# Performance work log

Measured on AMD Instinct MI355X. Metric: run time of the kernel, lower is better.

## Reference

```python
import jax, jax.numpy as jnp
import numpy as np

B = 16        # number of lists
N = 1024      # items per list (all equal)
D = 256       # feature dim (= dim_emb, need_embedding=False)


def setup_inputs() -> dict:
    key = jax.random.key(0)
    k1, k2, k3 = jax.random.split(key, 3)
    feats = jax.random.normal(k1, (B * N, D), dtype=jnp.float32)
    length = jnp.full((B,), N, dtype=jnp.int32)
    # Bilinear params: torch nn.Bilinear(d, d, 1) -> weight [1, d, d], bias [1]
    # xavier_uniform on the 3-d weight: bound = sqrt(6 / (fan_in + fan_out)) with
    # fan_in = d (last dim), fan_out = 1*d (per torch _calculate_fan_in_and_fan_out)
    bound = float(np.sqrt(6.0 / (D + D)))
    W_upper = jax.random.uniform(k2, (1, D, D), jnp.float32, -bound, bound)
    W_lower = jax.random.uniform(k3, (1, D, D), jnp.float32, -bound, bound)
    b_upper = jnp.zeros((1,), jnp.float32)
    b_lower = jnp.zeros((1,), jnp.float32)
    return {"feats": feats, "W_upper": W_upper, "b_upper": b_upper,
            "W_lower": W_lower, "b_lower": b_lower, "length": length}


def reference(feats, W_upper, b_upper, W_lower, b_lower, length):
    # nb_layers=0, need_embedding=False -> embedding and transformer are Identity.
    b = length.shape[0]
    n = feats.shape[0] // b  # equal-length lists -> static reshape
    d = feats.shape[-1]
    X = feats.reshape(b, n, d)  # [B, n, d]
    # For list i: repeated_feats_1 row (p*n + q) = x_p, repeated_feats_2 row = x_q,
    # so adjacency[p, q] = x_p^T W x_q + bias  (Bilinear with out=1).
    upper = jnp.einsum('bnd,de,bme->bnm', X, W_upper[0], X) + b_upper[0]
    lower = jnp.einsum('bnd,de,bme->bnm', X, W_lower[0], X) + b_lower[0]
    adj = jnp.triu(upper) + jnp.tril(lower, -1)  # [B, n, n]
    return adj
```

## Files before the change

kernel.cpp:

```cpp
#include <hip/hip_runtime.h>

#define BL 16
#define NL 1024
#define DD 256
#define KSTEPS 8

typedef short bf16x8 __attribute__((ext_vector_type(8)));
typedef float f32x4 __attribute__((ext_vector_type(4)));

static __device__ __forceinline__ short f32_to_bf16(float f) {
  union { float f; unsigned u; } v; v.f = f;
  unsigned r = (v.u + 0x7FFFu + ((v.u >> 16) & 1u)) >> 16;
  return (short)r;
}

static __device__ __forceinline__ void g2l16(const short* g, short* l) {
  __builtin_amdgcn_global_load_lds(
      (const __attribute__((address_space(1))) void*)g,
      (__attribute__((address_space(3))) void*)l, 16, 0, 0);
}


static __device__ __forceinline__ void stage_tile(const short* __restrict__ gbase,
                                                  short* __restrict__ lds,
                                                  int t, int k0) {
  const int row = t >> 2, kc = t & 3;
#pragma unroll
  for (int i = 0; i < 2; ++i) {
    const short* g = gbase + (size_t)(row + 64 * i) * DD + k0 + kc * 8;
    g2l16(g, lds + i * 2048 + t * 8);
  }
}

static __device__ __forceinline__ void mma_step(const short* __restrict__ As,
                                                const short* __restrict__ Bs,
                                                int wm, int wn, int r, int quad,
                                                f32x4 acc[4][4]) {
  const int ch = (quad ^ ((r >> 1) & 3)) * 8;
  bf16x8 af[4], bf[4];
#pragma unroll
  for (int i = 0; i < 4; ++i) {
    af[i] = *(const bf16x8*)(As + (wm + i * 16 + r) * 32 + ch);
    bf[i] = *(const bf16x8*)(Bs + (wn + i * 16 + r) * 32 + ch);
  }
#pragma unroll
  for (int mt = 0; mt < 4; ++mt)
#pragma unroll
    for (int nt = 0; nt < 4; ++nt)
      acc[mt][nt] = __builtin_amdgcn_mfma_f32_16x16x32_bf16(af[mt], bf[nt], acc[mt][nt], 0, 0, 0);
}

static __device__ __forceinline__ size_t sw_off(int row, int k) {
  const int panel = k >> 5, c = (k >> 3) & 3, j = k & 7;
  const int s = (row >> 1) & 3;
  return (size_t)row * DD + panel * 32 + ((c ^ s) * 8) + j;
}

__global__ __launch_bounds__(256) void k_prep(const float* __restrict__ X,
                                              const float* __restrict__ Wu,
                                              const float* __restrict__ Wl,
                                              short* __restrict__ Xb,
                                              short* __restrict__ WTu,
                                              short* __restrict__ WTl) {
  const int bid = blockIdx.x;
  if (bid < 2048) {
    const int i = bid * 256 + threadIdx.x;
    const int row = i >> 5, c32 = i & 31;
    const int panel = c32 >> 2, c = c32 & 3;
    const float4* src = (const float4*)(X + (size_t)row * DD + panel * 32 + c * 8);
    const float4 v0 = src[0], v1 = src[1];
    short o[8] = {f32_to_bf16(v0.x), f32_to_bf16(v0.y), f32_to_bf16(v0.z), f32_to_bf16(v0.w),
                  f32_to_bf16(v1.x), f32_to_bf16(v1.y), f32_to_bf16(v1.z), f32_to_bf16(v1.w)};
    const int s = (row >> 1) & 3;
    *(bf16x8*)(Xb + (size_t)row * DD + panel * 32 + ((c ^ s) * 8)) = *(bf16x8*)o;
  } else {
    const int id = bid - 2048;
    const int z = id >> 8, d = id & 255;
    const float* W = z ? Wl : Wu;
    short* WT = z ? WTl : WTu;
    const int e = threadIdx.x;
    WT[sw_off(e, d)] = f32_to_bf16(W[d * DD + e]);
  }
}

__global__ __launch_bounds__(256) void k_stage1(const short* __restrict__ Xb,
                                                const short* __restrict__ WTu,
                                                const short* __restrict__ WTl,
                                                short* __restrict__ YU,
                                                short* __restrict__ YL) {
  __shared__ short As[2][128 * 32], Bs[2][128 * 32];
  const short* Bt = blockIdx.z ? WTl : WTu;
  short* Y = blockIdx.z ? YL : YU;
  const int m0 = blockIdx.y * 128, n0 = blockIdx.x * 128;
  const int t = threadIdx.x, lane = t & 63, wave = t >> 6;
  const int r = lane & 15, quad = lane >> 4;
  const int wm = (wave >> 1) * 64, wn = (wave & 1) * 64;
  f32x4 acc[4][4] = {};
  const short* Ag = Xb + (size_t)m0 * DD;
  const short* Bg = Bt + (size_t)n0 * DD;
  stage_tile(Ag, As[0], t, 0);
  stage_tile(Bg, Bs[0], t, 0);
  for (int i = 0; i < KSTEPS; ++i) {
    __syncthreads();
    if (i + 1 < KSTEPS) {
      stage_tile(Ag, As[(i + 1) & 1], t, (i + 1) * 32);
      stage_tile(Bg, Bs[(i + 1) & 1], t, (i + 1) * 32);
    }
    mma_step(As[i & 1], Bs[i & 1], wm, wn, r, quad, acc);
  }
#pragma unroll
  for (int mt = 0; mt < 4; ++mt)
#pragma unroll
    for (int nt = 0; nt < 4; ++nt)
#pragma unroll
      for (int i = 0; i < 4; ++i)
        Y[sw_off(m0 + wm + mt * 16 + quad * 4 + i, n0 + wn + nt * 16 + r)] =
            f32_to_bf16(acc[mt][nt][i]);
}

__global__ __launch_bounds__(256) void k_stage2(const short* __restrict__ Xb,
                                                const short* __restrict__ YU,
                                                const short* __restrict__ YL,
                                                const float* __restrict__ bu_p,
                                                const float* __restrict__ bl_p,
                                                float* __restrict__ out) {
  __shared__ short As[2][128 * 32], Bs[2][128 * 32];
  const int pt = blockIdx.x >> 3, qt = blockIdx.x & 7, b = blockIdx.y;
  const size_t off = (size_t)b * NL * DD;
  const short* Bg = Xb + off + (size_t)qt * 128 * DD;
  const int t = threadIdx.x, lane = t & 63, wave = t >> 6;
  const int r = lane & 15, quad = lane >> 4;
  const int wm = (wave >> 1) * 64, wn = (wave & 1) * 64;
  float* Ob = out + (size_t)b * NL * NL;
  const int p0 = pt * 128 + wm, q0 = qt * 128 + wn;
  const float bu = bu_p[0], bl = bl_p[0];
  const bool diag = (pt == qt);
  const int npass = diag ? 2 : 1;

  for (int pass = 0; pass < npass; ++pass) {
    const bool useU = diag ? (pass == 0) : (qt > pt);
    const short* Ag = (useU ? YU : YL) + off + (size_t)pt * 128 * DD;
    const float bias = useU ? bu : bl;
    const f32x4 binit = {bias, bias, bias, bias};
    f32x4 acc[4][4];
#pragma unroll
    for (int mt = 0; mt < 4; ++mt)
#pragma unroll
      for (int nt = 0; nt < 4; ++nt) acc[mt][nt] = binit;

    __syncthreads();
    stage_tile(Ag, As[0], t, 0);
    stage_tile(Bg, Bs[0], t, 0);
    for (int i = 0; i < KSTEPS; ++i) {
      __syncthreads();
      if (i + 1 < KSTEPS) {
        stage_tile(Ag, As[(i + 1) & 1], t, (i + 1) * 32);
        stage_tile(Bg, Bs[(i + 1) & 1], t, (i + 1) * 32);
      }
      mma_step(As[i & 1], Bs[i & 1], wm, wn, r, quad, acc);
    }
#pragma unroll
    for (int mt = 0; mt < 4; ++mt)
#pragma unroll
      for (int nt = 0; nt < 4; ++nt)
#pragma unroll
        for (int i = 0; i < 4; ++i) {
          const int p = p0 + mt * 16 + quad * 4 + i;
          const int q = q0 + nt * 16 + r;
          if (!diag || (pass == 0 ? (q >= p) : (q < p)))
            Ob[(size_t)p * NL + q] = acc[mt][nt][i];
        }
  }
}

extern "C" void kernel_launch(void* const* d_in, const int* in_sizes, int n_in,
                              void* d_out, int out_size, void* d_ws, size_t ws_size,
                              hipStream_t stream) {
  const float* feats = (const float*)d_in[0];
  const float* Wu    = (const float*)d_in[1];
  const float* bu    = (const float*)d_in[2];
  const float* Wl    = (const float*)d_in[3];
  const float* bl    = (const float*)d_in[4];
  float* out = (float*)d_out;

  char* ws = (char*)d_ws;
  short* Xb  = (short*)(ws);
  short* YU  = (short*)(ws + (size_t)8 * 1024 * 1024);
  short* YL  = (short*)(ws + (size_t)16 * 1024 * 1024);
  short* WTu = (short*)(ws + (size_t)24 * 1024 * 1024);
  short* WTl = (short*)(ws + (size_t)24 * 1024 * 1024 + DD * DD * 2);

  k_prep<<<2048 + 512, 256, 0, stream>>>(feats, Wu, Wl, Xb, WTu, WTl);

  k_stage1<<<dim3(DD / 128, BL * NL / 128, 2), 256, 0, stream>>>(Xb, WTu, WTl, YU, YL);

  k_stage2<<<dim3(64, BL), 256, 0, stream>>>(Xb, YU, YL, bu, bl, out);
}
```

Before: 139.0 us.

## Pre-pack operands in MFMA fragment order and drop LDS staging

The prep kernel now writes X and the transposed W into a fragment-major layout (16-row strips, 32-wide k panels, lane-ordered 16-byte chunks). Each wave can then load its MFMA operands straight from global memory with coalesced vector loads, using register double-buffering instead of LDS tiles and __syncthreads. Stage 1 writes Y in the same packed layout, and stage 2 gives each wave an independent 64x64 output tile. This removes LDS traffic and barriers but loses operand sharing across waves, so each wave reloads its own A/B data from global memory or cache.

```diff
diff --git a/kernel.cpp b/kernel.cpp
--- a/kernel.cpp
+++ b/kernel.cpp
@@ -3,7 +3,6 @@
 #define BL 16
 #define NL 1024
 #define DD 256
-#define KSTEPS 8
 
 typedef short bf16x8 __attribute__((ext_vector_type(8)));
 typedef float f32x4 __attribute__((ext_vector_type(4)));
@@ -14,151 +13,122 @@
   return (short)r;
 }
 
-static __device__ __forceinline__ void g2l16(const short* g, short* l) {
-  __builtin_amdgcn_global_load_lds(
-      (const __attribute__((address_space(1))) void*)g,
-      (__attribute__((address_space(3))) void*)l, 16, 0, 0);
+
+static __device__ __forceinline__ void load4(const short* __restrict__ base,
+                                             int p, int l, bf16x8 f[4]) {
+#pragma unroll
+  for (int i = 0; i < 4; ++i)
+    f[i] = *(const bf16x8*)(base + i * 4096 + p * 512 + l * 8);
 }
 
-
-static __device__ __forceinline__ void stage_tile(const short* __restrict__ gbase,
-                                                  short* __restrict__ lds,
-                                                  int t, int k0) {
-  const int row = t >> 2, kc = t & 3;
+static __device__ __forceinline__ void gemm64(const short* __restrict__ Ab,
+                                              const short* __restrict__ Bb,
+                                              int l, f32x4 acc[4][4]) {
+  bf16x8 a[2][4], b[2][4];
+  load4(Ab, 0, l, a[0]);
+  load4(Bb, 0, l, b[0]);
 #pragma unroll
-  for (int i = 0; i < 2; ++i) {
-    const short* g = gbase + (size_t)(row + 64 * i) * DD + k0 + kc * 8;
-    g2l16(g, lds + i * 2048 + t * 8);
+  for (int p = 0; p < 8; ++p) {
+    if (p + 1 < 8) {
+      load4(Ab, p + 1, l, a[(p + 1) & 1]);
+      load4(Bb, p + 1, l, b[(p + 1) & 1]);
+    }
+#pragma unroll
+    for (int mt = 0; mt < 4; ++mt)
+#pragma unroll
+      for (int nt = 0; nt < 4; ++nt)
+        acc[mt][nt] = __builtin_amdgcn_mfma_f32_16x16x32_bf16(
+            a[p & 1][mt], b[p & 1][nt], acc[mt][nt], 0, 0, 0);
   }
-}
-
-static __device__ __forceinline__ void mma_step(const short* __restrict__ As,
-                                                const short* __restrict__ Bs,
-                                                int wm, int wn, int r, int quad,
-                                                f32x4 acc[4][4]) {
-  const int ch = (quad ^ ((r >> 1) & 3)) * 8;
-  bf16x8 af[4], bf[4];
-#pragma unroll
-  for (int i = 0; i < 4; ++i) {
-    af[i] = *(const bf16x8*)(As + (wm + i * 16 + r) * 32 + ch);
-    bf[i] = *(const bf16x8*)(Bs + (wn + i * 16 + r) * 32 + ch);
-  }
-#pragma unroll
-  for (int mt = 0; mt < 4; ++mt)
-#pragma unroll
-    for (int nt = 0; nt < 4; ++nt)
-      acc[mt][nt] = __builtin_amdgcn_mfma_f32_16x16x32_bf16(af[mt], bf[nt], acc[mt][nt], 0, 0, 0);
-}
-
-static __device__ __forceinline__ size_t sw_off(int row, int k) {
-  const int panel = k >> 5, c = (k >> 3) & 3, j = k & 7;
-  const int s = (row >> 1) & 3;
-  return (size_t)row * DD + panel * 32 + ((c ^ s) * 8) + j;
 }
 
 __global__ __launch_bounds__(256) void k_prep(const float* __restrict__ X,
                                               const float* __restrict__ Wu,
                                               const float* __restrict__ Wl,
-                                              short* __restrict__ Xb,
+                                              short* __restrict__ Xf,
                                               short* __restrict__ WTu,
                                               short* __restrict__ WTl) {
-  const int bid = blockIdx.x;
-  if (bid < 2048) {
-    const int i = bid * 256 + threadIdx.x;
-    const int row = i >> 5, c32 = i & 31;
-    const int panel = c32 >> 2, c = c32 & 3;
-    const float4* src = (const float4*)(X + (size_t)row * DD + panel * 32 + c * 8);
+  const int tid = blockIdx.x * 256 + threadIdx.x;
+  if (tid < BL * NL * 32) {
+    const int strip = tid >> 9, rest = tid & 511;
+    const int p = rest >> 6, l = rest & 63;
+    const int row = strip * 16 + (l & 15), k0 = p * 32 + (l >> 4) * 8;
+    const float4* src = (const float4*)(X + (size_t)row * DD + k0);
     const float4 v0 = src[0], v1 = src[1];
     short o[8] = {f32_to_bf16(v0.x), f32_to_bf16(v0.y), f32_to_bf16(v0.z), f32_to_bf16(v0.w),
                   f32_to_bf16(v1.x), f32_to_bf16(v1.y), f32_to_bf16(v1.z), f32_to_bf16(v1.w)};
-    const int s = (row >> 1) & 3;
-    *(bf16x8*)(Xb + (size_t)row * DD + panel * 32 + ((c ^ s) * 8)) = *(bf16x8*)o;
+    *(bf16x8*)(Xf + (size_t)strip * 4096 + p * 512 + l * 8) = *(bf16x8*)o;
   } else {
-    const int id = bid - 2048;
-    const int z = id >> 8, d = id & 255;
+    const int g = tid - BL * NL * 32;
+    const int z = g >> 13, rest = g & 8191;
+    const int strip = rest >> 9, rest2 = rest & 511;
+    const int p = rest2 >> 6, l = rest2 & 63;
+    const int e = strip * 16 + (l & 15), d0 = p * 32 + (l >> 4) * 8;
     const float* W = z ? Wl : Wu;
     short* WT = z ? WTl : WTu;
-    const int e = threadIdx.x;
-    WT[sw_off(e, d)] = f32_to_bf16(W[d * DD + e]);
+    short o[8];
+#pragma unroll
+    for (int j = 0; j < 8; ++j) o[j] = f32_to_bf16(W[(size_t)(d0 + j) * DD + e]);
+    *(bf16x8*)(WT + (size_t)strip * 4096 + p * 512 + l * 8) = *(bf16x8*)o;
   }
 }
 
-__global__ __launch_bounds__(256) void k_stage1(const short* __restrict__ Xb,
+__global__ __launch_bounds__(256) void k_stage1(const short* __restrict__ Xf,
                                                 const short* __restrict__ WTu,
                                                 const short* __restrict__ WTl,
                                                 short* __restrict__ YU,
                                                 short* __restrict__ YL) {
-  __shared__ short As[2][128 * 32], Bs[2][128 * 32];
-  const short* Bt = blockIdx.z ? WTl : WTu;
-  short* Y = blockIdx.z ? YL : YU;
-  const int m0 = blockIdx.y * 128, n0 = blockIdx.x * 128;
-  const int t = threadIdx.x, lane = t & 63, wave = t >> 6;
-  const int r = lane & 15, quad = lane >> 4;
-  const int wm = (wave >> 1) * 64, wn = (wave & 1) * 64;
+  const int w = threadIdx.x >> 6, l = threadIdx.x & 63;
+  const int quad = l >> 4, rcol = l & 15;
+  const short* WT = blockIdx.y ? WTl : WTu;
+  short* Y = blockIdx.y ? YL : YU;
+  const short* Ab = Xf + (size_t)blockIdx.x * 4 * 4096;
+  const short* Bb = WT + (size_t)w * 4 * 4096;
   f32x4 acc[4][4] = {};
-  const short* Ag = Xb + (size_t)m0 * DD;
-  const short* Bg = Bt + (size_t)n0 * DD;
-  stage_tile(Ag, As[0], t, 0);
-  stage_tile(Bg, Bs[0], t, 0);
-  for (int i = 0; i < KSTEPS; ++i) {
-    __syncthreads();
-    if (i + 1 < KSTEPS) {
-      stage_tile(Ag, As[(i + 1) & 1], t, (i + 1) * 32);
-      stage_tile(Bg, Bs[(i + 1) & 1], t, (i + 1) * 32);
-    }
-    mma_step(As[i & 1], Bs[i & 1], wm, wn, r, quad, acc);
-  }
+  gemm64(Ab, Bb, l, acc);
 #pragma unroll
   for (int mt = 0; mt < 4; ++mt)
 #pragma unroll
-    for (int nt = 0; nt < 4; ++nt)
+    for (int nt = 0; nt < 4; ++nt) {
+      const int nk = w * 64 + nt * 16 + rcol;
+      short* base = Y + (size_t)(blockIdx.x * 4 + mt) * 4096 + (nk >> 5) * 512 +
+                    ((nk >> 3) & 3) * 128 + (nk & 7);
 #pragma unroll
       for (int i = 0; i < 4; ++i)
-        Y[sw_off(m0 + wm + mt * 16 + quad * 4 + i, n0 + wn + nt * 16 + r)] =
-            f32_to_bf16(acc[mt][nt][i]);
+        base[(quad * 4 + i) * 8] = f32_to_bf16(acc[mt][nt][i]);
+    }
 }
 
-__global__ __launch_bounds__(256) void k_stage2(const short* __restrict__ Xb,
+__global__ __launch_bounds__(256) void k_stage2(const short* __restrict__ Xf,
                                                 const short* __restrict__ YU,
                                                 const short* __restrict__ YL,
                                                 const float* __restrict__ bu_p,
                                                 const float* __restrict__ bl_p,
                                                 float* __restrict__ out) {
-  __shared__ short As[2][128 * 32], Bs[2][128 * 32];
-  const int pt = blockIdx.x >> 3, qt = blockIdx.x & 7, b = blockIdx.y;
-  const size_t off = (size_t)b * NL * DD;
-  const short* Bg = Xb + off + (size_t)qt * 128 * DD;
-  const int t = threadIdx.x, lane = t & 63, wave = t >> 6;
-  const int r = lane & 15, quad = lane >> 4;
-  const int wm = (wave >> 1) * 64, wn = (wave & 1) * 64;
+  const int w = threadIdx.x >> 6, l = threadIdx.x & 63;
+  const int quad = l >> 4, rcol = l & 15;
+  const int qt = blockIdx.x & 15, pb = blockIdx.x >> 4;
+  const int b = blockIdx.y;
+  const int pti = pb * 4 + w;
+  const size_t loff = (size_t)b * NL * DD;
+  const short* Bb = Xf + loff + (size_t)qt * 4 * 4096;
   float* Ob = out + (size_t)b * NL * NL;
-  const int p0 = pt * 128 + wm, q0 = qt * 128 + wn;
+  const int p0 = pti * 64, q0 = qt * 64;
   const float bu = bu_p[0], bl = bl_p[0];
-  const bool diag = (pt == qt);
+  const bool diag = (pti == qt);
   const int npass = diag ? 2 : 1;
 
   for (int pass = 0; pass < npass; ++pass) {
-    const bool useU = diag ? (pass == 0) : (qt > pt);
-    const short* Ag = (useU ? YU : YL) + off + (size_t)pt * 128 * DD;
+    const bool useU = diag ? (pass == 0) : (qt > pti);
     const float bias = useU ? bu : bl;
+    const short* Ab = (useU ? YU : YL) + loff + (size_t)pti * 4 * 4096;
     const f32x4 binit = {bias, bias, bias, bias};
     f32x4 acc[4][4];
 #pragma unroll
     for (int mt = 0; mt < 4; ++mt)
 #pragma unroll
       for (int nt = 0; nt < 4; ++nt) acc[mt][nt] = binit;
-
-    __syncthreads();
-    stage_tile(Ag, As[0], t, 0);
-    stage_tile(Bg, Bs[0], t, 0);
-    for (int i = 0; i < KSTEPS; ++i) {
-      __syncthreads();
-      if (i + 1 < KSTEPS) {
-        stage_tile(Ag, As[(i + 1) & 1], t, (i + 1) * 32);
-        stage_tile(Bg, Bs[(i + 1) & 1], t, (i + 1) * 32);
-      }
-      mma_step(As[i & 1], Bs[i & 1], wm, wn, r, quad, acc);
-    }
+    gemm64(Ab, Bb, l, acc);
 #pragma unroll
     for (int mt = 0; mt < 4; ++mt)
 #pragma unroll
@@ -166,7 +136,7 @@
 #pragma unroll
         for (int i = 0; i < 4; ++i) {
           const int p = p0 + mt * 16 + quad * 4 + i;
-          const int q = q0 + nt * 16 + r;
+          const int q = q0 + nt * 16 + rcol;
           if (!diag || (pass == 0 ? (q >= p) : (q < p)))
             Ob[(size_t)p * NL + q] = acc[mt][nt][i];
         }
@@ -184,15 +154,15 @@
   float* out = (float*)d_out;
 
   char* ws = (char*)d_ws;
-  short* Xb  = (short*)(ws);
+  short* Xf  = (short*)(ws);
   short* YU  = (short*)(ws + (size_t)8 * 1024 * 1024);
   short* YL  = (short*)(ws + (size_t)16 * 1024 * 1024);
   short* WTu = (short*)(ws + (size_t)24 * 1024 * 1024);
   short* WTl = (short*)(ws + (size_t)24 * 1024 * 1024 + DD * DD * 2);
 
-  k_prep<<<2048 + 512, 256, 0, stream>>>(feats, Wu, Wl, Xb, WTu, WTl);
+  k_prep<<<(BL * NL * 32 + 16384) / 256, 256, 0, stream>>>(feats, Wu, Wl, Xf, WTu, WTl);
 
-  k_stage1<<<dim3(DD / 128, BL * NL / 128, 2), 256, 0, stream>>>(Xb, WTu, WTl, YU, YL);
+  k_stage1<<<dim3(BL * NL / 64, 2), 256, 0, stream>>>(Xf, WTu, WTl, YU, YL);
 
-  k_stage2<<<dim3(64, BL), 256, 0, stream>>>(Xb, YU, YL, bu, bl, out);
+  k_stage2<<<dim3(64, BL), 256, 0, stream>>>(Xf, YU, YL, bu, bl, out);
 }
```

Result: slower. 188.9 us (+35.9%).
